# Kernel optimization log

Hardware: AMD Instinct MI355X
Metric: run time of the kernel (lower is better)

Reference implementation:

```python
import jax, jax.numpy as jnp
import numpy as np

B = 2048       # batch
F_IN = 1024    # input feature dim
R_EMB = 1024   # rows of EmbedLinear sparse weight (new features)
NNZ_E = 65536  # nnz of embed sparse weight
F_OUT = 1024   # output dim of ExpandingLinear
NNZ_W = 131072 # nnz of main sparse weight [F_OUT, F_IN + R_EMB]
NNZ_B = 512    # nnz of sparse bias
F_MID = F_IN + R_EMB


def setup_inputs() -> dict:
    key = jax.random.key(0)
    ks = jax.random.split(key, 9)
    return {
        "x": jax.random.normal(ks[0], (B, F_IN), jnp.float32),
        "embed_rows": jax.random.randint(ks[1], (NNZ_E,), 0, R_EMB, jnp.int32),
        "embed_cols": jax.random.randint(ks[2], (NNZ_E,), 0, F_IN, jnp.int32),
        "embed_vals": jax.random.normal(ks[3], (NNZ_E,), jnp.float32) * 0.05,
        "w_rows": jax.random.randint(ks[4], (NNZ_W,), 0, F_OUT, jnp.int32),
        "w_cols": jax.random.randint(ks[5], (NNZ_W,), 0, F_MID, jnp.int32),
        "w_vals": jax.random.normal(ks[6], (NNZ_W,), jnp.float32) * 0.05,
        "bias_idx": jax.random.randint(ks[7], (NNZ_B,), 0, F_OUT, jnp.int32),
        "bias_vals": jax.random.normal(ks[8], (NNZ_B,), jnp.float32),
    }


def _spmm(rows, cols, vals, x, n_rows):
    # sparse COO [n_rows, F] @ x.T -> transposed: returns [B, n_rows]
    # (matches torch.sparse.mm(sparse_w, input.t()).t())
    g = vals[:, None] * x.T[cols]                              # [nnz, B] gather + scale
    return jax.ops.segment_sum(g, rows, num_segments=n_rows).T # scatter-add over rows


def reference(x, embed_rows, embed_cols, embed_vals,
              w_rows, w_cols, w_vals, bias_idx, bias_vals):
    # EmbedLinear.forward: sparse mm + ReLU + concat along features
    h = jax.nn.relu(_spmm(embed_rows, embed_cols, embed_vals, x, R_EMB))  # [B, R_EMB]
    x2 = jnp.concatenate([x, h], axis=1)                                   # [B, F_MID]
    # ExpandingLinear tail: sparse weight mm + densified sparse bias
    bias = jnp.zeros((F_OUT,), x.dtype).at[bias_idx].add(bias_vals)
    return _spmm(w_rows, w_cols, w_vals, x2, F_OUT) + bias[None, :]        # [B, F_OUT]
```

## Files before the change

kernel.cpp:

```cpp
#include <hip/hip_runtime.h>
#include <hip/hip_bf16.h>

#define B_SZ   2048
#define F_IN   1024
#define R_EMB  1024
#define F_OUT  1024
#define F_MID  2048
#define NNZ_E  65536
#define NNZ_W  131072
#define NNZ_B  512

typedef __bf16 bf16x8 __attribute__((ext_vector_type(8)));
typedef float  f32x4  __attribute__((ext_vector_type(4)));

__device__ inline void gload16(const void* g, void* l) {
    __builtin_amdgcn_global_load_lds(
        (const __attribute__((address_space(1))) void*)g,
        (__attribute__((address_space(3))) void*)l, 16, 0, 0);
}

__device__ inline ushort f2bf(float v) {
    __hip_bfloat16 h = __float2bfloat16(v);
    return *reinterpret_cast<ushort*>(&h);
}

__global__ void k_zero4(float4* __restrict__ p, int n) {
    int i = blockIdx.x * blockDim.x + threadIdx.x;
    if (i < n) p[i] = make_float4(0.f, 0.f, 0.f, 0.f);
}

__global__ void k_scatter_fused(const int* __restrict__ er, const int* __restrict__ ec,
                                const float* __restrict__ ev,
                                const int* __restrict__ wr_, const int* __restrict__ wc_,
                                const float* __restrict__ wv,
                                const int* __restrict__ bi, const float* __restrict__ bv,
                                float* __restrict__ Ef, float* __restrict__ Wf,
                                float* __restrict__ biasd) {
    int b = blockIdx.x, t = threadIdx.x;
    if (b < NNZ_E / 256) {
        int i = b * 256 + t;
        atomicAdd(&Ef[(size_t)er[i] * F_IN + ec[i]], ev[i]);
    } else if (b < NNZ_E / 256 + NNZ_W / 256) {
        int i = (b - NNZ_E / 256) * 256 + t;
        atomicAdd(&Wf[(size_t)wr_[i] * F_MID + wc_[i]], wv[i]);
    } else {
        int i = t;
        atomicAdd(&biasd[bi[i]], bv[i]);
        i += 256;
        atomicAdd(&biasd[bi[i]], bv[i]);
    }
}

__global__ void k_cvt_fused(const float4* __restrict__ x, ushort* __restrict__ x2,
                            const float4* __restrict__ Ef, ushort* __restrict__ Ebf,
                            const float4* __restrict__ Wf, ushort* __restrict__ Wbf) {
    int b = blockIdx.x, t = threadIdx.x;
    if (b < 2048) {
        int i = b * 256 + t;
        int row = i >> 8, c4 = i & 255;
        float4 v = x[i];
        ((ushort4*)x2)[(size_t)row * (F_MID / 4) + c4] =
            make_ushort4(f2bf(v.x), f2bf(v.y), f2bf(v.z), f2bf(v.w));
    } else if (b < 3072) {
        int i = (b - 2048) * 256 + t;
        float4 v = Ef[i];
        ((ushort4*)Ebf)[i] = make_ushort4(f2bf(v.x), f2bf(v.y), f2bf(v.z), f2bf(v.w));
    } else {
        int i = (b - 3072) * 256 + t;
        float4 v = Wf[i];
        ((ushort4*)Wbf)[i] = make_ushort4(f2bf(v.x), f2bf(v.y), f2bf(v.z), f2bf(v.w));
    }
}

template <int PHASE>
__global__ __launch_bounds__(256)
void k_gemm3(const ushort* __restrict__ x2,
             const ushort* __restrict__ Ebf,
             const ushort* __restrict__ Wbf,
             const float* __restrict__ biasd,
             float* __restrict__ out,
             ushort* __restrict__ hOut)
{
    constexpr int BS = 64, BK = 64, NT = 1024 / BK;
    __shared__ ushort lds[2][2][BS * BK];
    const int tid = threadIdx.x;
    const int w = tid >> 6, l = tid & 63;
    const int wr = w >> 1, wc = w & 1;
    const int la = l & 15;
    const int m0 = blockIdx.x * BS;

    int mode, ldb, n0;
    const ushort* A;
    const ushort* Bm;
    if (PHASE == 0) {
        if (blockIdx.y < 16) {
            mode = 0; A = x2;        Bm = Ebf;        ldb = F_IN;  n0 = blockIdx.y * BS;
        } else {
            mode = 1; A = x2;        Bm = Wbf;        ldb = F_MID; n0 = (blockIdx.y - 16) * BS;
        }
    } else {
        mode = 2;     A = x2 + F_IN; Bm = Wbf + F_IN; ldb = F_MID; n0 = blockIdx.y * BS;
    }

    const int srow = w * 8 + (l >> 3);
    const int ldst = w * 512 + l * 8;

    f32x4 acc[2][2] = {};

    #define STAGE(buf, k0)                                                        \
        _Pragma("unroll")                                                         \
        for (int i = 0; i < 2; ++i) {                                             \
            int row = i * 32 + srow;                                              \
            int scol = (k0) + ((((l & 7) ^ (row & 7))) << 3);                     \
            gload16(A  + (size_t)(m0 + row) * F_MID + scol,                       \
                    &lds[buf][0][i * 2048 + ldst]);                               \
            gload16(Bm + (size_t)(n0 + row) * ldb + scol,                         \
                    &lds[buf][1][i * 2048 + ldst]);                               \
        }

    auto compute = [&](int cur) {
        const ushort* sA = &lds[cur][0][0];
        const ushort* sB = &lds[cur][1][0];
        #pragma unroll
        for (int ks = 0; ks < 2; ++ks) {
            const int k8 = ks * 4 + (l >> 4);
            bf16x8 af[2], bg[2];
            #pragma unroll
            for (int m = 0; m < 2; ++m) {
                int row = wr * 32 + m * 16 + la;
                af[m] = *(const bf16x8*)(sA + row * BK + ((k8 ^ (row & 7)) << 3));
            }
            #pragma unroll
            for (int n = 0; n < 2; ++n) {
                int row = wc * 32 + n * 16 + la;
                bg[n] = *(const bf16x8*)(sB + row * BK + ((k8 ^ (row & 7)) << 3));
            }
            #pragma unroll
            for (int m = 0; m < 2; ++m)
                #pragma unroll
                for (int n = 0; n < 2; ++n)
                    acc[m][n] = __builtin_amdgcn_mfma_f32_16x16x32_bf16(
                        af[m], bg[n], acc[m][n], 0, 0, 0);
        }
    };

    STAGE(0, 0);

    for (int t = 0; t < NT - 1; ++t) {
        STAGE((t + 1) & 1, (t + 1) * BK);
        asm volatile("s_waitcnt vmcnt(4)" ::: "memory");
        __builtin_amdgcn_s_barrier();
        __builtin_amdgcn_sched_barrier(0);
        compute(t & 1);
        __builtin_amdgcn_sched_barrier(0);
        __builtin_amdgcn_s_barrier();
    }
    asm volatile("s_waitcnt vmcnt(0)" ::: "memory");
    __builtin_amdgcn_s_barrier();
    __builtin_amdgcn_sched_barrier(0);
    compute((NT - 1) & 1);
    #undef STAGE

    const int lr = (l >> 4) * 4;
    #pragma unroll
    for (int m = 0; m < 2; ++m) {
        #pragma unroll
        for (int n = 0; n < 2; ++n) {
            const int col = n0 + wc * 32 + n * 16 + la;
            if (mode == 0) {
                #pragma unroll
                for (int j = 0; j < 4; ++j) {
                    int row = m0 + wr * 32 + m * 16 + lr + j;
                    hOut[(size_t)row * F_MID + col] = f2bf(fmaxf(acc[m][n][j], 0.f));
                }
            } else if (mode == 1) {
                const float bv = biasd[col];
                #pragma unroll
                for (int j = 0; j < 4; ++j) {
                    int row = m0 + wr * 32 + m * 16 + lr + j;
                    out[(size_t)row * F_OUT + col] = acc[m][n][j] + bv;
                }
            } else {
                #pragma unroll
                for (int j = 0; j < 4; ++j) {
                    int row = m0 + wr * 32 + m * 16 + lr + j;
                    out[(size_t)row * F_OUT + col] += acc[m][n][j];
                }
            }
        }
    }
}

extern "C" void kernel_launch(void* const* d_in, const int* in_sizes, int n_in,
                              void* d_out, int out_size, void* d_ws, size_t ws_size,
                              hipStream_t stream) {
    const float* x          = (const float*)d_in[0];
    const int*   embed_rows = (const int*)  d_in[1];
    const int*   embed_cols = (const int*)  d_in[2];
    const float* embed_vals = (const float*)d_in[3];
    const int*   w_rows     = (const int*)  d_in[4];
    const int*   w_cols     = (const int*)  d_in[5];
    const float* w_vals     = (const float*)d_in[6];
    const int*   bias_idx   = (const int*)  d_in[7];
    const float* bias_vals  = (const float*)d_in[8];
    float* out = (float*)d_out;

    char* ws = (char*)d_ws;
    ushort* x2    = (ushort*)ws;
    float*  Wf    = (float*)(ws + (8u << 20));
    float*  Ef    = (float*)(ws + (16u << 20));
    float*  biasd = (float*)(ws + (20u << 20));
    ushort* Ebf   = (ushort*)(ws + (20u << 20) + 4096);
    ushort* Wbf   = (ushort*)(ws + (22u << 20) + 4096);

    k_zero4<<<3073, 256, 0, stream>>>((float4*)(ws + (8u << 20)), 786688);

    k_scatter_fused<<<NNZ_E / 256 + NNZ_W / 256 + 1, 256, 0, stream>>>(
        embed_rows, embed_cols, embed_vals,
        w_rows, w_cols, w_vals,
        bias_idx, bias_vals, Ef, Wf, biasd);

    k_cvt_fused<<<5120, 256, 0, stream>>>((const float4*)x, x2,
                                          (const float4*)Ef, Ebf,
                                          (const float4*)Wf, Wbf);

    k_gemm3<0><<<dim3(B_SZ / 64, 32), 256, 0, stream>>>(
        x2, Ebf, Wbf, biasd, out, x2 + F_IN);

    k_gemm3<1><<<dim3(B_SZ / 64, 16), 256, 0, stream>>>(
        x2, Ebf, Wbf, biasd, out, x2 + F_IN);
}
```

Measured before the change: 55.29 us.

## Enlarge GEMM tiles to 128x128 and split-K phase 1 with atomic accumulation

The two GEMM phases now use 128x128 output tiles with a 4x4 MFMA grid per wave instead of 64x64, so each loaded A/B tile is reused across more MFMAs and global traffic per FLOP falls. Phase 1 is split along K into two halves of 512, keeping its grid at 256 blocks, and its results are added into the output with atomic adds instead of read-modify-write. The price is fewer blocks in phase 0 (occupancy on 256 CUs), higher register and LDS use per block, and nondeterministic float summation order from the atomics.

After: 73.41 us. 32.8% more time.

```diff
diff --git a/kernel.cpp b/kernel.cpp
--- a/kernel.cpp
+++ b/kernel.cpp
@@ -74,81 +74,86 @@
 
 template <int PHASE>
 __global__ __launch_bounds__(256)
-void k_gemm3(const ushort* __restrict__ x2,
-             const ushort* __restrict__ Ebf,
-             const ushort* __restrict__ Wbf,
-             const float* __restrict__ biasd,
-             float* __restrict__ out,
-             ushort* __restrict__ hOut)
+void k_gemm128(const ushort* __restrict__ x2,
+               const ushort* __restrict__ Ebf,
+               const ushort* __restrict__ Wbf,
+               const float* __restrict__ biasd,
+               float* __restrict__ out,
+               ushort* __restrict__ hOut)
 {
-    constexpr int BS = 64, BK = 64, NT = 1024 / BK;
-    __shared__ ushort lds[2][2][BS * BK];
+    constexpr int BK = 64;
+    constexpr int NT = (PHASE == 0) ? 16 : 8;
+    __shared__ ushort lA[2][128 * BK];
+    __shared__ ushort lB[2][128 * BK];
     const int tid = threadIdx.x;
     const int w = tid >> 6, l = tid & 63;
     const int wr = w >> 1, wc = w & 1;
-    const int la = l & 15;
-    const int m0 = blockIdx.x * BS;
-
-    int mode, ldb, n0;
+    const int la = l & 15, lg = l >> 4;
+    const int m0 = blockIdx.x * 128;
+    const int by = blockIdx.y;
+
+    int mode, n0, kbase = 0, ldb;
+    const ushort* Bm;
     const ushort* A;
-    const ushort* Bm;
     if (PHASE == 0) {
-        if (blockIdx.y < 16) {
-            mode = 0; A = x2;        Bm = Ebf;        ldb = F_IN;  n0 = blockIdx.y * BS;
-        } else {
-            mode = 1; A = x2;        Bm = Wbf;        ldb = F_MID; n0 = (blockIdx.y - 16) * BS;
+        if (by < 8) { mode = 0; A = x2;        Bm = Ebf;        ldb = F_IN;  n0 = by * 128; }
+        else        { mode = 1; A = x2;        Bm = Wbf;        ldb = F_MID; n0 = (by - 8) * 128; }
+    } else {
+        mode = 2;     A = x2 + F_IN; Bm = Wbf + F_IN; ldb = F_MID;
+        n0 = (by & 7) * 128; kbase = (by >> 3) * 512;
+    }
+
+    const int srow = tid >> 3, sslot = tid & 7;
+
+    f32x4 acc[4][4] = {};
+
+    #define STAGE(buf, k0)                                                      \
+        _Pragma("unroll")                                                       \
+        for (int i = 0; i < 4; ++i) {                                           \
+            int row = i * 32 + srow;                                            \
+            int col = (k0) + ((sslot ^ (row & 7)) << 3);                        \
+            gload16(A + (size_t)(m0 + row) * F_MID + col,                       \
+                    &lA[buf][i * 2048 + tid * 8]);                              \
+        }                                                                       \
+        _Pragma("unroll")                                                       \
+        for (int i = 0; i < 4; ++i) {                                           \
+            int row = i * 32 + srow;                                            \
+            int col = (k0) + ((sslot ^ (row & 7)) << 3);                        \
+            gload16(Bm + (size_t)(n0 + row) * ldb + col,                        \
+                    &lB[buf][i * 2048 + tid * 8]);                              \
         }
-    } else {
-        mode = 2;     A = x2 + F_IN; Bm = Wbf + F_IN; ldb = F_MID; n0 = blockIdx.y * BS;
-    }
-
-    const int srow = w * 8 + (l >> 3);
-    const int ldst = w * 512 + l * 8;
-
-    f32x4 acc[2][2] = {};
-
-    #define STAGE(buf, k0)                                                        \
-        _Pragma("unroll")                                                         \
-        for (int i = 0; i < 2; ++i) {                                             \
-            int row = i * 32 + srow;                                              \
-            int scol = (k0) + ((((l & 7) ^ (row & 7))) << 3);                     \
-            gload16(A  + (size_t)(m0 + row) * F_MID + scol,                       \
-                    &lds[buf][0][i * 2048 + ldst]);                               \
-            gload16(Bm + (size_t)(n0 + row) * ldb + scol,                         \
-                    &lds[buf][1][i * 2048 + ldst]);                               \
-        }
 
     auto compute = [&](int cur) {
-        const ushort* sA = &lds[cur][0][0];
-        const ushort* sB = &lds[cur][1][0];
+        const ushort* sA = &lA[cur][0];
+        const ushort* sB = &lB[cur][0];
         #pragma unroll
         for (int ks = 0; ks < 2; ++ks) {
-            const int k8 = ks * 4 + (l >> 4);
-            bf16x8 af[2], bg[2];
+            const int c = ks * 4 + lg;
+            bf16x8 af[4], bg[4];
             #pragma unroll
-            for (int m = 0; m < 2; ++m) {
-                int row = wr * 32 + m * 16 + la;
-                af[m] = *(const bf16x8*)(sA + row * BK + ((k8 ^ (row & 7)) << 3));
+            for (int m = 0; m < 4; ++m) {
+                int row = wr * 64 + m * 16 + la;
+                af[m] = *(const bf16x8*)(sA + row * BK + ((c ^ (row & 7)) << 3));
             }
             #pragma unroll
-            for (int n = 0; n < 2; ++n) {
-                int row = wc * 32 + n * 16 + la;
-                bg[n] = *(const bf16x8*)(sB + row * BK + ((k8 ^ (row & 7)) << 3));
+            for (int n = 0; n < 4; ++n) {
+                int row = wc * 64 + n * 16 + la;
+                bg[n] = *(const bf16x8*)(sB + row * BK + ((c ^ (row & 7)) << 3));
             }
             #pragma unroll
-            for (int m = 0; m < 2; ++m)
-                #pragma unroll
-                for (int n = 0; n < 2; ++n)
+            for (int m = 0; m < 4; ++m)
+                #pragma unroll
+                for (int n = 0; n < 4; ++n)
                     acc[m][n] = __builtin_amdgcn_mfma_f32_16x16x32_bf16(
                         af[m], bg[n], acc[m][n], 0, 0, 0);
         }
     };
 
-    STAGE(0, 0);
+    STAGE(0, kbase);
 
     for (int t = 0; t < NT - 1; ++t) {
-        STAGE((t + 1) & 1, (t + 1) * BK);
-        asm volatile("s_waitcnt vmcnt(4)" ::: "memory");
+        STAGE((t + 1) & 1, kbase + (t + 1) * BK);
+        asm volatile("s_waitcnt vmcnt(8)" ::: "memory");
         __builtin_amdgcn_s_barrier();
         __builtin_amdgcn_sched_barrier(0);
         compute(t & 1);
@@ -161,30 +166,30 @@
     compute((NT - 1) & 1);
     #undef STAGE
 
-    const int lr = (l >> 4) * 4;
+    const int lr = lg * 4;
     #pragma unroll
-    for (int m = 0; m < 2; ++m) {
+    for (int m = 0; m < 4; ++m) {
         #pragma unroll
-        for (int n = 0; n < 2; ++n) {
-            const int col = n0 + wc * 32 + n * 16 + la;
+        for (int n = 0; n < 4; ++n) {
+            const int col = n0 + wc * 64 + n * 16 + la;
             if (mode == 0) {
                 #pragma unroll
                 for (int j = 0; j < 4; ++j) {
-                    int row = m0 + wr * 32 + m * 16 + lr + j;
+                    int row = m0 + wr * 64 + m * 16 + lr + j;
                     hOut[(size_t)row * F_MID + col] = f2bf(fmaxf(acc[m][n][j], 0.f));
                 }
             } else if (mode == 1) {
                 const float bv = biasd[col];
                 #pragma unroll
                 for (int j = 0; j < 4; ++j) {
-                    int row = m0 + wr * 32 + m * 16 + lr + j;
+                    int row = m0 + wr * 64 + m * 16 + lr + j;
                     out[(size_t)row * F_OUT + col] = acc[m][n][j] + bv;
                 }
             } else {
                 #pragma unroll
                 for (int j = 0; j < 4; ++j) {
-                    int row = m0 + wr * 32 + m * 16 + lr + j;
-                    out[(size_t)row * F_OUT + col] += acc[m][n][j];
+                    int row = m0 + wr * 64 + m * 16 + lr + j;
+                    unsafeAtomicAdd(&out[(size_t)row * F_OUT + col], acc[m][n][j]);
                 }
             }
         }
@@ -224,9 +229,9 @@
                                           (const float4*)Ef, Ebf,
                                           (const float4*)Wf, Wbf);
 
-    k_gemm3<0><<<dim3(B_SZ / 64, 32), 256, 0, stream>>>(
+    k_gemm128<0><<<dim3(B_SZ / 128, 16), 256, 0, stream>>>(
         x2, Ebf, Wbf, biasd, out, x2 + F_IN);
 
-    k_gemm3<1><<<dim3(B_SZ / 64, 16), 256, 0, stream>>>(
+    k_gemm128<1><<<dim3(B_SZ / 128, 16), 256, 0, stream>>>(
         x2, Ebf, Wbf, biasd, out, x2 + F_IN);
 }
```
